# Optimization experiments

Measured on AMD Instinct MI355X. Metric: run time of the kernel, lower is better.

Reference implementation:

```python
import jax, jax.numpy as jnp
import numpy as np

N = 16384        # tokens (batch*seq)
D_MODEL = 4096
D_HALF = D_MODEL // 2
NUM_EXPERTS = 64
TOP_K = 4
SCALE = 2.0


def setup_inputs() -> dict:
    key = jax.random.key(0)
    k_u, k_ex, k_ey = jax.random.split(key, 3)
    u = jax.random.normal(k_u, (N, D_MODEL), dtype=jnp.float32)
    E_x = jax.random.normal(k_ex, (D_HALF, NUM_EXPERTS), dtype=jnp.float32) * 0.01
    E_y = jax.random.normal(k_ey, (D_HALF, NUM_EXPERTS), dtype=jnp.float32) * 0.01
    bias = jnp.zeros((NUM_EXPERTS,), dtype=jnp.float32)
    # torus-shape scalar parameters (torch init values)
    c = jnp.float32(2.0)
    d = jnp.float32(2.0)
    a1 = jnp.float32(4.0)
    b1 = jnp.float32(4.0)
    return {"u": u, "E_x": E_x, "E_y": E_y, "bias": bias,
            "c": c, "d": d, "a1": a1, "b1": b1, "top_k": TOP_K}


def reference(u, E_x, E_y, bias, c, d, a1, b1, top_k):
    d_half = E_x.shape[0]
    num_experts = E_x.shape[1]
    # dual small GEMM + tanh squash onto [-scale, scale]
    x = jnp.tanh(u[..., :d_half] @ E_x) * SCALE        # [N, E]
    y = jnp.tanh(u[..., d_half:] @ E_y) * SCALE        # [N, E]
    xa, ya = jnp.abs(x), jnp.abs(y)
    # 4CM torus: f(x,y) = (|x|^a1 + |y|^b1) * exp(-(|x|^c + |y|^d))
    scores = (xa ** a1 + ya ** b1) * jnp.exp(-(xa ** c + ya ** d)) + bias
    topk_s, topk_i = jax.lax.top_k(scores, top_k)       # [N, k]
    probs = jax.nn.softmax(scores, axis=-1)             # [N, E]
    aux_loss = jnp.sum(jnp.mean(probs, axis=0) ** 2) * num_experts
    return topk_i, topk_s, scores, aux_loss
```

## Files before the change

kernel.cpp:

```cpp
#include <hip/hip_runtime.h>
#include <math.h>
#include <stdint.h>

#define N_TOK 16384
#define DM    4096
#define DH    2048
#define NE    64
#define TBE   64
#define TOPK  4
#define NST   16

#define OFF_TI  0
#define OFF_TS  (N_TOK * TOPK)
#define OFF_SC  (N_TOK * TOPK * 2)
#define OFF_AUX (N_TOK * TOPK * 2 + N_TOK * NE)

typedef __attribute__((ext_vector_type(4)))  float  f32x4;
typedef __attribute__((ext_vector_type(16))) float  f32x16;
typedef __attribute__((ext_vector_type(8)))  __bf16 bf16x8;
typedef __attribute__((ext_vector_type(8)))  unsigned short u16x8;

#define BSPLIT_ELEMS (2 * 64 * 3 * 2 * 2 * 64 * 8)
#define PRE_BYTE_OFF (2u * 1024u * 1024u)

__device__ __forceinline__ void split3(float a, __bf16& h, __bf16& m, __bf16& l) {
    h = (__bf16)a;
    float r = a - (float)h;
    m = (__bf16)r;
    float r2 = r - (float)m;
    l = (__bf16)r2;
}

__device__ __forceinline__ void stage16(const float* g, void* l) {
    __builtin_amdgcn_global_load_lds(
        (const __attribute__((address_space(1))) unsigned int*)(uintptr_t)g,
        (__attribute__((address_space(3))) unsigned int*)(uintptr_t)l,
        16, 0, 0);
}

__device__ __forceinline__ void splitPair(const f32x4& lo, const f32x4& hi,
                                          u16x8& sh, u16x8& sm, u16x8& sl) {
    #pragma unroll
    for (int q = 0; q < 2; ++q)
        #pragma unroll
        for (int j = 0; j < 4; ++j) {
            float a = (q == 0 ? lo : hi)[j];
            unsigned h32 = __float_as_uint(a) & 0xFFFF0000u;
            float rr = a - __uint_as_float(h32);
            unsigned m32 = __float_as_uint(rr) & 0xFFFF0000u;
            float r2f = rr - __uint_as_float(m32);
            sh[q * 4 + j] = (unsigned short)(h32 >> 16);
            sm[q * 4 + j] = (unsigned short)(m32 >> 16);
            sl[q * 4 + j] = (unsigned short)(__float_as_uint(r2f) >> 16);
        }
}

__global__ __launch_bounds__(256) void prep_B(
    const float* __restrict__ Ex, const float* __restrict__ Ey,
    __bf16* __restrict__ Bws)
{
    const int t    = blockIdx.x * 256 + threadIdx.x;
    const int lane = t & 63;
    const int sk   = (t >> 6) & 1;
    const int et   = (t >> 7) & 1;
    const int ks   = (t >> 8) & 63;
    const int h    = (t >> 14) & 1;
    const float* E = h ? Ey : Ex;
    const int e  = et * 32 + (lane & 31);
    const int k0 = ks * 32 + sk * 16 + (lane >> 5) * 8;
    bf16x8 vh, vm, vl;
    #pragma unroll
    for (int j = 0; j < 8; ++j) {
        __bf16 hh, mm, ll;
        split3(E[(size_t)(k0 + j) * NE + e], hh, mm, ll);
        vh[j] = hh; vm[j] = mm; vl[j] = ll;
    }
    #pragma unroll
    for (int s = 0; s < 3; ++s) {
        size_t base = ((((((size_t)h * 64 + ks) * 3 + s) * 2 + et) * 2 + sk) * 64 + lane) * 8;
        *(bf16x8*)(Bws + base) = (s == 0) ? vh : (s == 1) ? vm : vl;
    }
}

__global__ __launch_bounds__(256, 1) void gemm_half(
    const float* __restrict__ u, const __bf16* __restrict__ Bws,
    float* __restrict__ pre)
{
    __shared__ __align__(16) unsigned char aring[4][2][16384];

    const int tid  = threadIdx.x;
    const int lane = tid & 63;
    const int wv   = tid >> 6;
    const int h    = blockIdx.x & 1;
    const int tile = blockIdx.x >> 1;
    const int t0   = tile * 128;
    const int lr   = lane & 31;
    const int lkh  = lane >> 5;
    const int hb   = lane >> 5;

    const float* uw = u + (size_t)(t0 + wv * 32 + hb) * DM + h * DH;
    const unsigned ldsW = (unsigned)(uintptr_t)(void*)&aring[wv][0][0];
    const char* bwsB = (const char*)Bws + (size_t)(h * 64) * 12288 + lane * 16;

    f32x16 acc0 = {}, acc1 = {};

    auto stageA = [&](int s, int slot) {
        const float* gb = uw + s * 128;
        unsigned char* d = &aring[wv][slot][0];
        #pragma unroll
        for (int i = 0; i < 16; ++i) {
            const int m = ((2 * i) & 7) | hb;
            const float* g = gb + (size_t)(2 * i) * DM + (((lane & 31) ^ m) * 4);
            stage16(g, d + i * 1024);
        }
    };

    stageA(0, 0);
    __builtin_amdgcn_sched_barrier(0);

    #pragma unroll 1
    for (int s = 0; s < NST; ++s) {
        f32x4 bb[4][12];
        #pragma unroll
        for (int c = 0; c < 4; ++c) {
            const char* bc = bwsB + (size_t)(s * 4 + c) * 12288;
            #pragma unroll
            for (int sp = 0; sp < 3; ++sp) {
                uint64_t ad = (uint64_t)(uintptr_t)(bc + sp * 4096);
                asm volatile(
                    "global_load_dwordx4 %0, %4, off\n\t"
                    "global_load_dwordx4 %1, %4, off offset:1024\n\t"
                    "global_load_dwordx4 %2, %4, off offset:2048\n\t"
                    "global_load_dwordx4 %3, %4, off offset:3072"
                    : "=&v"(bb[c][sp * 4 + 0]), "=&v"(bb[c][sp * 4 + 1]),
                      "=&v"(bb[c][sp * 4 + 2]), "=&v"(bb[c][sp * 4 + 3])
                    : "v"(ad));
            }
        }
        __builtin_amdgcn_sched_barrier(0);
        asm volatile("s_waitcnt vmcnt(48)" ::: "memory");
        __builtin_amdgcn_sched_barrier(0);
        stageA(s + 1 < NST ? s + 1 : NST - 1, (s + 1) & 1);
        __builtin_amdgcn_sched_barrier(0);

        const unsigned ab = ldsW + (unsigned)((s & 1) * 16384) + (unsigned)lr * 512;
        const unsigned xr = (unsigned)(lr & 7);
        #pragma unroll
        for (int c = 0; c < 4; ++c) {
            const unsigned a = (unsigned)(c * 8 + lkh * 2);
            unsigned ad0 = ab + (((a    ) ^ xr) << 4);
            unsigned ad1 = ab + (((a + 1) ^ xr) << 4);
            unsigned ad2 = ab + (((a + 4) ^ xr) << 4);
            unsigned ad3 = ab + (((a + 5) ^ xr) << 4);
            f32x4 r0, r1, r2, r3;
            asm volatile(
                "ds_read_b128 %0, %4\n\t"
                "ds_read_b128 %1, %5\n\t"
                "ds_read_b128 %2, %6\n\t"
                "ds_read_b128 %3, %7\n\t"
                "s_waitcnt lgkmcnt(0)"
                : "=&v"(r0), "=&v"(r1), "=&v"(r2), "=&v"(r3)
                : "v"(ad0), "v"(ad1), "v"(ad2), "v"(ad3));
            __builtin_amdgcn_sched_barrier(0);
            u16x8 sh0, sm0, sl0, sh1, sm1, sl1;
            splitPair(r0, r1, sh0, sm0, sl0);
            splitPair(r2, r3, sh1, sm1, sl1);
            __builtin_amdgcn_sched_barrier(0);
            if      (c == 0) asm volatile("s_waitcnt vmcnt(52)" ::: "memory");
            else if (c == 1) asm volatile("s_waitcnt vmcnt(40)" ::: "memory");
            else if (c == 2) asm volatile("s_waitcnt vmcnt(28)" ::: "memory");
            else             asm volatile("s_waitcnt vmcnt(16)" ::: "memory");
            __builtin_amdgcn_sched_barrier(0);
            {
                bf16x8 vh = __builtin_bit_cast(bf16x8, sh0);
                bf16x8 vm = __builtin_bit_cast(bf16x8, sm0);
                bf16x8 vl = __builtin_bit_cast(bf16x8, sl0);
                bf16x8 Bh = __builtin_bit_cast(bf16x8, bb[c][0]);
                bf16x8 Bm = __builtin_bit_cast(bf16x8, bb[c][4]);
                bf16x8 Bl = __builtin_bit_cast(bf16x8, bb[c][8]);
                acc0 = __builtin_amdgcn_mfma_f32_32x32x16_bf16(vh, Bh, acc0, 0, 0, 0);
                acc0 = __builtin_amdgcn_mfma_f32_32x32x16_bf16(vm, Bh, acc0, 0, 0, 0);
                acc0 = __builtin_amdgcn_mfma_f32_32x32x16_bf16(vl, Bh, acc0, 0, 0, 0);
                acc0 = __builtin_amdgcn_mfma_f32_32x32x16_bf16(vh, Bm, acc0, 0, 0, 0);
                acc0 = __builtin_amdgcn_mfma_f32_32x32x16_bf16(vm, Bm, acc0, 0, 0, 0);
                acc0 = __builtin_amdgcn_mfma_f32_32x32x16_bf16(vh, Bl, acc0, 0, 0, 0);
                Bh = __builtin_bit_cast(bf16x8, bb[c][2]);
                Bm = __builtin_bit_cast(bf16x8, bb[c][6]);
                Bl = __builtin_bit_cast(bf16x8, bb[c][10]);
                acc1 = __builtin_amdgcn_mfma_f32_32x32x16_bf16(vh, Bh, acc1, 0, 0, 0);
                acc1 = __builtin_amdgcn_mfma_f32_32x32x16_bf16(vm, Bh, acc1, 0, 0, 0);
                acc1 = __builtin_amdgcn_mfma_f32_32x32x16_bf16(vl, Bh, acc1, 0, 0, 0);
                acc1 = __builtin_amdgcn_mfma_f32_32x32x16_bf16(vh, Bm, acc1, 0, 0, 0);
                acc1 = __builtin_amdgcn_mfma_f32_32x32x16_bf16(vm, Bm, acc1, 0, 0, 0);
                acc1 = __builtin_amdgcn_mfma_f32_32x32x16_bf16(vh, Bl, acc1, 0, 0, 0);
            }
            {
                bf16x8 vh = __builtin_bit_cast(bf16x8, sh1);
                bf16x8 vm = __builtin_bit_cast(bf16x8, sm1);
                bf16x8 vl = __builtin_bit_cast(bf16x8, sl1);
                bf16x8 Bh = __builtin_bit_cast(bf16x8, bb[c][1]);
                bf16x8 Bm = __builtin_bit_cast(bf16x8, bb[c][5]);
                bf16x8 Bl = __builtin_bit_cast(bf16x8, bb[c][9]);
                acc0 = __builtin_amdgcn_mfma_f32_32x32x16_bf16(vh, Bh, acc0, 0, 0, 0);
                acc0 = __builtin_amdgcn_mfma_f32_32x32x16_bf16(vm, Bh, acc0, 0, 0, 0);
                acc0 = __builtin_amdgcn_mfma_f32_32x32x16_bf16(vl, Bh, acc0, 0, 0, 0);
                acc0 = __builtin_amdgcn_mfma_f32_32x32x16_bf16(vh, Bm, acc0, 0, 0, 0);
                acc0 = __builtin_amdgcn_mfma_f32_32x32x16_bf16(vm, Bm, acc0, 0, 0, 0);
                acc0 = __builtin_amdgcn_mfma_f32_32x32x16_bf16(vh, Bl, acc0, 0, 0, 0);
                Bh = __builtin_bit_cast(bf16x8, bb[c][3]);
                Bm = __builtin_bit_cast(bf16x8, bb[c][7]);
                Bl = __builtin_bit_cast(bf16x8, bb[c][11]);
                acc1 = __builtin_amdgcn_mfma_f32_32x32x16_bf16(vh, Bh, acc1, 0, 0, 0);
                acc1 = __builtin_amdgcn_mfma_f32_32x32x16_bf16(vm, Bh, acc1, 0, 0, 0);
                acc1 = __builtin_amdgcn_mfma_f32_32x32x16_bf16(vl, Bh, acc1, 0, 0, 0);
                acc1 = __builtin_amdgcn_mfma_f32_32x32x16_bf16(vh, Bm, acc1, 0, 0, 0);
                acc1 = __builtin_amdgcn_mfma_f32_32x32x16_bf16(vm, Bm, acc1, 0, 0, 0);
                acc1 = __builtin_amdgcn_mfma_f32_32x32x16_bf16(vh, Bl, acc1, 0, 0, 0);
            }
            __builtin_amdgcn_sched_barrier(0);
        }
    }

    float* dst = pre + (((size_t)h * N_TOK) + t0 + wv * 32) * NE + lr;
    #pragma unroll
    for (int q = 0; q < 4; ++q)
        #pragma unroll
        for (int j = 0; j < 4; ++j) {
            const int row = j + 8 * q + 4 * lkh;
            dst[(size_t)row * NE]      = acc0[q * 4 + j];
            dst[(size_t)row * NE + 32] = acc1[q * 4 + j];
        }
}

__global__ __launch_bounds__(256) void torus_ep(
    const float* __restrict__ pre, const float* __restrict__ bias,
    const float* __restrict__ cp, const float* __restrict__ dp,
    const float* __restrict__ a1p, const float* __restrict__ b1p,
    float* __restrict__ out, float* __restrict__ esum)
{
    __shared__ float stile[TBE][NE + 1];
    __shared__ float s_m[TBE], s_inv[TBE];

    const int tid = threadIdx.x;
    const int t0  = blockIdx.x * TBE;

    {
        const float c_ = *cp, d_ = *dp, a1_ = *a1p, b1_ = *b1p;
        const int tok = tid >> 2;
        const int e0  = (tid & 3) * 16;
        const float* px = pre + (size_t)(t0 + tok) * NE + e0;
        const float* py = pre + ((size_t)N_TOK + t0 + tok) * NE + e0;
        #pragma unroll
        for (int i = 0; i < 16; i += 4) {
            f32x4 xv = *(const f32x4*)(px + i);
            f32x4 yv = *(const f32x4*)(py + i);
            #pragma unroll
            for (int j = 0; j < 4; ++j) {
                int e = e0 + i + j;
                float x = tanhf(xv[j]) * 2.0f;
                float y = tanhf(yv[j]) * 2.0f;
                float xa = fabsf(x), ya = fabsf(y);
                float sc = (powf(xa, a1_) + powf(ya, b1_)) *
                           expf(-(powf(xa, c_) + powf(ya, d_))) + bias[e];
                stile[tok][e] = sc;
            }
        }
    }
    __syncthreads();

    if (tid < TBE) {
        const int t = tid;
        float bv[TOPK]; int bi[TOPK];
        #pragma unroll
        for (int p = 0; p < TOPK; ++p) {
            float best = -INFINITY; int besti = 0;
            for (int e = 0; e < NE; ++e) {
                float v = stile[t][e];
                bool taken = false;
                #pragma unroll
                for (int q = 0; q < p; ++q) taken = taken || (bi[q] == e);
                if (!taken && v > best) { best = v; besti = e; }
            }
            bv[p] = best; bi[p] = besti;
        }
        const float m = bv[0];
        float denom = 0.0f;
        for (int e = 0; e < NE; ++e) denom += expf(stile[t][e] - m);
        const float inv = 1.0f / denom;
        s_m[t] = m; s_inv[t] = inv;
        #pragma unroll
        for (int p = 0; p < TOPK; ++p) {
            out[OFF_TI + (size_t)(t0 + t) * TOPK + p] = (float)bi[p];
            out[OFF_TS + (size_t)(t0 + t) * TOPK + p] = bv[p];
        }
    }
    __syncthreads();

    if (tid < NE) {
        const int e = tid;
        float cs = 0.0f;
        for (int t = 0; t < TBE; ++t)
            cs += expf(stile[t][e] - s_m[t]) * s_inv[t];
        atomicAdd(&esum[e], cs);
    }

    for (int idx = tid; idx < TBE * NE; idx += 256)
        out[OFF_SC + (size_t)t0 * NE + idx] = stile[idx >> 6][idx & (NE - 1)];
}

__global__ __launch_bounds__(64) void torus_aux(const float* __restrict__ esum,
                                                float* __restrict__ out)
{
    const int e = threadIdx.x;
    float s = esum[e] * (1.0f / (float)N_TOK);
    float v = s * s;
    #pragma unroll
    for (int off = 32; off > 0; off >>= 1) v += __shfl_down(v, off);
    if (e == 0) out[OFF_AUX] = v * (float)NE;
}

extern "C" void kernel_launch(void* const* d_in, const int* in_sizes, int n_in,
                              void* d_out, int out_size, void* d_ws, size_t ws_size,
                              hipStream_t stream) {
    const float* u    = (const float*)d_in[0];
    const float* Ex   = (const float*)d_in[1];
    const float* Ey   = (const float*)d_in[2];
    const float* bias = (const float*)d_in[3];
    const float* cp   = (const float*)d_in[4];
    const float* dp   = (const float*)d_in[5];
    const float* a1p  = (const float*)d_in[6];
    const float* b1p  = (const float*)d_in[7];
    float* out  = (float*)d_out;
    __bf16* Bws = (__bf16*)d_ws;
    float* esum = (float*)((char*)d_ws + (size_t)BSPLIT_ELEMS * sizeof(__bf16));
    float* pre  = (float*)((char*)d_ws + PRE_BYTE_OFF);

    prep_B<<<128, 256, 0, stream>>>(Ex, Ey, Bws);
    hipMemsetAsync(esum, 0, NE * sizeof(float), stream);
    gemm_half<<<N_TOK / 128 * 2, 256, 0, stream>>>(u, Bws, pre);
    torus_ep<<<N_TOK / TBE, 256, 0, stream>>>(pre, bias, cp, dp, a1p, b1p, out, esum);
    torus_aux<<<1, 64, 0, stream>>>(esum, out);
}
```

Measured before the change: 127.5 us.

## Stage shared B weights through LDS cooperatively and fold esum memset into prep

The GEMM kernel now stages the split-bf16 B tiles into a double-buffered LDS ring cooperatively across all four waves, rather than each wave loading its own copy of the whole B slice into registers from global memory. The K step is halved (more stages, smaller A tiles) to fit the new LDS budget, and a block-wide barrier with a full vmcnt wait is added each stage. The esum zeroing moves into prep_B, which drops one memset launch. The change cuts redundant global/L2 traffic for B and register pressure, but adds a barrier and a full wait per stage that may reduce overlap.

```diff
diff --git a/kernel.cpp b/kernel.cpp
--- a/kernel.cpp
+++ b/kernel.cpp
@@ -8,7 +8,7 @@
 #define NE    64
 #define TBE   64
 #define TOPK  4
-#define NST   16
+#define NST   32
 
 #define OFF_TI  0
 #define OFF_TS  (N_TOK * TOPK)
@@ -57,8 +57,9 @@
 
 __global__ __launch_bounds__(256) void prep_B(
     const float* __restrict__ Ex, const float* __restrict__ Ey,
-    __bf16* __restrict__ Bws)
+    __bf16* __restrict__ Bws, float* __restrict__ esum)
 {
+    if (blockIdx.x == 0 && threadIdx.x < NE) esum[threadIdx.x] = 0.0f;
     const int t    = blockIdx.x * 256 + threadIdx.x;
     const int lane = t & 63;
     const int sk   = (t >> 6) & 1;
@@ -86,7 +87,8 @@
     const float* __restrict__ u, const __bf16* __restrict__ Bws,
     float* __restrict__ pre)
 {
-    __shared__ __align__(16) unsigned char aring[4][2][16384];
+    __shared__ __align__(16) unsigned char aring[4][2][8192];
+    __shared__ __align__(16) unsigned char bring[2][24576];
 
     const int tid  = threadIdx.x;
     const int lane = tid & 63;
@@ -96,97 +98,102 @@
     const int t0   = tile * 128;
     const int lr   = lane & 31;
     const int lkh  = lane >> 5;
-    const int hb   = lane >> 5;
-
-    const float* uw = u + (size_t)(t0 + wv * 32 + hb) * DM + h * DH;
-    const unsigned ldsW = (unsigned)(uintptr_t)(void*)&aring[wv][0][0];
-    const char* bwsB = (const char*)Bws + (size_t)(h * 64) * 12288 + lane * 16;
+
+    const float* abase = u + (size_t)(t0 + wv * 32) * DM + h * DH;
+    const char* bsrc = (const char*)Bws + (size_t)h * 64 * 12288
+                     + (size_t)(wv >> 1) * 12288 + (size_t)((wv & 1) * 6) * 1024 + lane * 16;
+
+    auto stageA = [&](int s, int slot) {
+        unsigned char* d = &aring[wv][slot][0];
+        const float* gs = abase + s * 64;
+        #pragma unroll
+        for (int i = 0; i < 8; ++i) {
+            const int r = i * 4 + (lane >> 4);
+            const int c = (lane & 15) ^ (r & 15);
+            stage16(gs + (size_t)r * DM + c * 4, d + i * 1024 + lane * 16);
+        }
+    };
+    auto stageB = [&](int s, int slot) {
+        unsigned char* d = &bring[slot][0] + (size_t)(wv * 6) * 1024;
+        const char* srcs = bsrc + (size_t)(2 * s) * 12288;
+        #pragma unroll
+        for (int j = 0; j < 6; ++j)
+            stage16((const float*)(srcs + j * 1024), d + j * 1024 + lane * 16);
+    };
 
     f32x16 acc0 = {}, acc1 = {};
-
-    auto stageA = [&](int s, int slot) {
-        const float* gb = uw + s * 128;
-        unsigned char* d = &aring[wv][slot][0];
-        #pragma unroll
-        for (int i = 0; i < 16; ++i) {
-            const int m = ((2 * i) & 7) | hb;
-            const float* g = gb + (size_t)(2 * i) * DM + (((lane & 31) ^ m) * 4);
-            stage16(g, d + i * 1024);
-        }
-    };
-
-    stageA(0, 0);
-    __builtin_amdgcn_sched_barrier(0);
+    const unsigned aB  = (unsigned)(uintptr_t)(void*)&aring[wv][0][0];
+    const unsigned bB  = (unsigned)(uintptr_t)(void*)&bring[0][0];
+    const unsigned swz = (unsigned)(lr & 15);
+
+    stageA(0, 0); stageB(0, 0);
 
     #pragma unroll 1
     for (int s = 0; s < NST; ++s) {
-        f32x4 bb[4][12];
-        #pragma unroll
-        for (int c = 0; c < 4; ++c) {
-            const char* bc = bwsB + (size_t)(s * 4 + c) * 12288;
-            #pragma unroll
-            for (int sp = 0; sp < 3; ++sp) {
-                uint64_t ad = (uint64_t)(uintptr_t)(bc + sp * 4096);
-                asm volatile(
-                    "global_load_dwordx4 %0, %4, off\n\t"
-                    "global_load_dwordx4 %1, %4, off offset:1024\n\t"
-                    "global_load_dwordx4 %2, %4, off offset:2048\n\t"
-                    "global_load_dwordx4 %3, %4, off offset:3072"
-                    : "=&v"(bb[c][sp * 4 + 0]), "=&v"(bb[c][sp * 4 + 1]),
-                      "=&v"(bb[c][sp * 4 + 2]), "=&v"(bb[c][sp * 4 + 3])
-                    : "v"(ad));
-            }
-        }
+        asm volatile("s_waitcnt vmcnt(0)" ::: "memory");
         __builtin_amdgcn_sched_barrier(0);
-        asm volatile("s_waitcnt vmcnt(48)" ::: "memory");
+        __builtin_amdgcn_s_barrier();
         __builtin_amdgcn_sched_barrier(0);
-        stageA(s + 1 < NST ? s + 1 : NST - 1, (s + 1) & 1);
+        if (s + 1 < NST) { stageA(s + 1, (s + 1) & 1); stageB(s + 1, (s + 1) & 1); }
         __builtin_amdgcn_sched_barrier(0);
 
-        const unsigned ab = ldsW + (unsigned)((s & 1) * 16384) + (unsigned)lr * 512;
-        const unsigned xr = (unsigned)(lr & 7);
-        #pragma unroll
-        for (int c = 0; c < 4; ++c) {
-            const unsigned a = (unsigned)(c * 8 + lkh * 2);
-            unsigned ad0 = ab + (((a    ) ^ xr) << 4);
-            unsigned ad1 = ab + (((a + 1) ^ xr) << 4);
-            unsigned ad2 = ab + (((a + 4) ^ xr) << 4);
-            unsigned ad3 = ab + (((a + 5) ^ xr) << 4);
+        const unsigned as = aB + (unsigned)((s & 1) * 8192) + (unsigned)lr * 256;
+        const unsigned bs = bB + (unsigned)((s & 1) * 24576);
+        #pragma unroll
+        for (int k2 = 0; k2 < 2; ++k2) {
+            const unsigned c0 = (unsigned)(k2 * 8 + lkh * 2);
+            unsigned a0 = as + (((c0    ) ^ swz) << 4);
+            unsigned a1 = as + (((c0 + 1) ^ swz) << 4);
+            unsigned a2 = as + (((c0 + 4) ^ swz) << 4);
+            unsigned a3 = as + (((c0 + 5) ^ swz) << 4);
             f32x4 r0, r1, r2, r3;
             asm volatile(
                 "ds_read_b128 %0, %4\n\t"
                 "ds_read_b128 %1, %5\n\t"
                 "ds_read_b128 %2, %6\n\t"
-                "ds_read_b128 %3, %7\n\t"
+                "ds_read_b128 %3, %7"
+                : "=&v"(r0), "=&v"(r1), "=&v"(r2), "=&v"(r3)
+                : "v"(a0), "v"(a1), "v"(a2), "v"(a3));
+            const unsigned bk = bs + (unsigned)(k2 * 12 * 1024) + (unsigned)lane * 16;
+            f32x4 b0,b1,b2,b3,b4,b5,b6,b7,b8,b9,b10,b11;
+            asm volatile(
+                "ds_read_b128 %0, %12 offset:0\n\t"
+                "ds_read_b128 %1, %12 offset:1024\n\t"
+                "ds_read_b128 %2, %12 offset:2048\n\t"
+                "ds_read_b128 %3, %12 offset:3072\n\t"
+                "ds_read_b128 %4, %12 offset:4096\n\t"
+                "ds_read_b128 %5, %12 offset:5120\n\t"
+                "ds_read_b128 %6, %12 offset:6144\n\t"
+                "ds_read_b128 %7, %12 offset:7168\n\t"
+                "ds_read_b128 %8, %12 offset:8192\n\t"
+                "ds_read_b128 %9, %12 offset:9216\n\t"
+                "ds_read_b128 %10, %12 offset:10240\n\t"
+                "ds_read_b128 %11, %12 offset:11264\n\t"
                 "s_waitcnt lgkmcnt(0)"
-                : "=&v"(r0), "=&v"(r1), "=&v"(r2), "=&v"(r3)
-                : "v"(ad0), "v"(ad1), "v"(ad2), "v"(ad3));
+                : "=&v"(b0), "=&v"(b1), "=&v"(b2), "=&v"(b3), "=&v"(b4), "=&v"(b5),
+                  "=&v"(b6), "=&v"(b7), "=&v"(b8), "=&v"(b9), "=&v"(b10), "=&v"(b11)
+                : "v"(bk));
             __builtin_amdgcn_sched_barrier(0);
             u16x8 sh0, sm0, sl0, sh1, sm1, sl1;
             splitPair(r0, r1, sh0, sm0, sl0);
             splitPair(r2, r3, sh1, sm1, sl1);
             __builtin_amdgcn_sched_barrier(0);
-            if      (c == 0) asm volatile("s_waitcnt vmcnt(52)" ::: "memory");
-            else if (c == 1) asm volatile("s_waitcnt vmcnt(40)" ::: "memory");
-            else if (c == 2) asm volatile("s_waitcnt vmcnt(28)" ::: "memory");
-            else             asm volatile("s_waitcnt vmcnt(16)" ::: "memory");
-            __builtin_amdgcn_sched_barrier(0);
             {
                 bf16x8 vh = __builtin_bit_cast(bf16x8, sh0);
                 bf16x8 vm = __builtin_bit_cast(bf16x8, sm0);
                 bf16x8 vl = __builtin_bit_cast(bf16x8, sl0);
-                bf16x8 Bh = __builtin_bit_cast(bf16x8, bb[c][0]);
-                bf16x8 Bm = __builtin_bit_cast(bf16x8, bb[c][4]);
-                bf16x8 Bl = __builtin_bit_cast(bf16x8, bb[c][8]);
+                bf16x8 Bh = __builtin_bit_cast(bf16x8, b0);
+                bf16x8 Bm = __builtin_bit_cast(bf16x8, b4);
+                bf16x8 Bl = __builtin_bit_cast(bf16x8, b8);
                 acc0 = __builtin_amdgcn_mfma_f32_32x32x16_bf16(vh, Bh, acc0, 0, 0, 0);
                 acc0 = __builtin_amdgcn_mfma_f32_32x32x16_bf16(vm, Bh, acc0, 0, 0, 0);
                 acc0 = __builtin_amdgcn_mfma_f32_32x32x16_bf16(vl, Bh, acc0, 0, 0, 0);
                 acc0 = __builtin_amdgcn_mfma_f32_32x32x16_bf16(vh, Bm, acc0, 0, 0, 0);
                 acc0 = __builtin_amdgcn_mfma_f32_32x32x16_bf16(vm, Bm, acc0, 0, 0, 0);
                 acc0 = __builtin_amdgcn_mfma_f32_32x32x16_bf16(vh, Bl, acc0, 0, 0, 0);
-                Bh = __builtin_bit_cast(bf16x8, bb[c][2]);
-                Bm = __builtin_bit_cast(bf16x8, bb[c][6]);
-                Bl = __builtin_bit_cast(bf16x8, bb[c][10]);
+                Bh = __builtin_bit_cast(bf16x8, b2);
+                Bm = __builtin_bit_cast(bf16x8, b6);
+                Bl = __builtin_bit_cast(bf16x8, b10);
                 acc1 = __builtin_amdgcn_mfma_f32_32x32x16_bf16(vh, Bh, acc1, 0, 0, 0);
                 acc1 = __builtin_amdgcn_mfma_f32_32x32x16_bf16(vm, Bh, acc1, 0, 0, 0);
                 acc1 = __builtin_amdgcn_mfma_f32_32x32x16_bf16(vl, Bh, acc1, 0, 0, 0);
@@ -198,18 +205,18 @@
                 bf16x8 vh = __builtin_bit_cast(bf16x8, sh1);
                 bf16x8 vm = __builtin_bit_cast(bf16x8, sm1);
                 bf16x8 vl = __builtin_bit_cast(bf16x8, sl1);
-                bf16x8 Bh = __builtin_bit_cast(bf16x8, bb[c][1]);
-                bf16x8 Bm = __builtin_bit_cast(bf16x8, bb[c][5]);
-                bf16x8 Bl = __builtin_bit_cast(bf16x8, bb[c][9]);
+                bf16x8 Bh = __builtin_bit_cast(bf16x8, b1);
+                bf16x8 Bm = __builtin_bit_cast(bf16x8, b5);
+                bf16x8 Bl = __builtin_bit_cast(bf16x8, b9);
                 acc0 = __builtin_amdgcn_mfma_f32_32x32x16_bf16(vh, Bh, acc0, 0, 0, 0);
                 acc0 = __builtin_amdgcn_mfma_f32_32x32x16_bf16(vm, Bh, acc0, 0, 0, 0);
                 acc0 = __builtin_amdgcn_mfma_f32_32x32x16_bf16(vl, Bh, acc0, 0, 0, 0);
                 acc0 = __builtin_amdgcn_mfma_f32_32x32x16_bf16(vh, Bm, acc0, 0, 0, 0);
                 acc0 = __builtin_amdgcn_mfma_f32_32x32x16_bf16(vm, Bm, acc0, 0, 0, 0);
                 acc0 = __builtin_amdgcn_mfma_f32_32x32x16_bf16(vh, Bl, acc0, 0, 0, 0);
-                Bh = __builtin_bit_cast(bf16x8, bb[c][3]);
-                Bm = __builtin_bit_cast(bf16x8, bb[c][7]);
-                Bl = __builtin_bit_cast(bf16x8, bb[c][11]);
+                Bh = __builtin_bit_cast(bf16x8, b3);
+                Bm = __builtin_bit_cast(bf16x8, b7);
+                Bl = __builtin_bit_cast(bf16x8, b11);
                 acc1 = __builtin_amdgcn_mfma_f32_32x32x16_bf16(vh, Bh, acc1, 0, 0, 0);
                 acc1 = __builtin_amdgcn_mfma_f32_32x32x16_bf16(vm, Bh, acc1, 0, 0, 0);
                 acc1 = __builtin_amdgcn_mfma_f32_32x32x16_bf16(vl, Bh, acc1, 0, 0, 0);
@@ -335,8 +342,7 @@
     float* esum = (float*)((char*)d_ws + (size_t)BSPLIT_ELEMS * sizeof(__bf16));
     float* pre  = (float*)((char*)d_ws + PRE_BYTE_OFF);
 
-    prep_B<<<128, 256, 0, stream>>>(Ex, Ey, Bws);
-    hipMemsetAsync(esum, 0, NE * sizeof(float), stream);
+    prep_B<<<128, 256, 0, stream>>>(Ex, Ey, Bws, esum);
     gemm_half<<<N_TOK / 128 * 2, 256, 0, stream>>>(u, Bws, pre);
     torus_ep<<<N_TOK / TBE, 256, 0, stream>>>(pre, bias, cp, dp, a1p, b1p, out, esum);
     torus_aux<<<1, 64, 0, stream>>>(esum, out);
```

Measured after the change: 120.6 us. 5.4% less time.
